# Optimization experiments

Measured on AMD Instinct MI355X. Metric: run time of the kernel, lower is better.

## Reference

```python
import jax, jax.numpy as jnp
import numpy as np
from jax import lax

DIM = 256
NUM_HEADS = 8
SW = 7
HEAD_DIM = DIM // NUM_HEADS
SCALE = HEAD_DIM ** -0.5


def setup_inputs() -> dict:
    key = jax.random.key(0)
    ks = jax.random.split(key, 7)
    B, C, H, W = 8, DIM, 56, 56
    x = jax.random.normal(ks[0], (B, C, H, W), dtype=jnp.float32)
    w_qkv = jax.random.normal(ks[1], (3 * C, C), dtype=jnp.float32) * 0.02
    b_qkv = jnp.zeros((3 * C,), dtype=jnp.float32)
    # depthwise 3x3 kernel, OIHW with feature_group_count=C -> (C,1,3,3)
    w_dw = jax.random.normal(ks[2], (C, 1, 3, 3), dtype=jnp.float32) * 0.02
    b_dw = jnp.zeros((C,), dtype=jnp.float32)
    w_proj = jax.random.normal(ks[3], (C, C), dtype=jnp.float32) * 0.02
    b_proj = jnp.zeros((C,), dtype=jnp.float32)
    return {"x": x, "w_qkv": w_qkv, "b_qkv": b_qkv, "w_dw": w_dw,
            "b_dw": b_dw, "w_proj": w_proj, "b_proj": b_proj}


def _conv1x1(x, w, b):
    # x:[B,C,H,W], w:[O,C] -> [B,O,H,W]
    return jnp.einsum('bchw,oc->bohw', x, w) + b[None, :, None, None]


def _dwconv3x3(x, w, b):
    C = x.shape[1]
    y = lax.conv_general_dilated(x, w, window_strides=(1, 1), padding='SAME',
                                 dimension_numbers=('NCHW', 'OIHW', 'NCHW'),
                                 feature_group_count=C)
    return y + b[None, :, None, None]


def _stripe_attn_H(q, k, v, sw):
    # q,k,v: [B,h,C,H,W]; local attention within sw-thick horizontal stripes
    B, h, C, H, W = q.shape
    sw = min(sw, H)
    pad = (-H) % sw
    if pad:
        pw = [(0, 0)] * 3 + [(0, pad), (0, 0)]
        q = jnp.pad(q, pw); k = jnp.pad(k, pw); v = jnp.pad(v, pw)
    Hp = H + pad
    n = Hp // sw

    def rs(t):
        # -> [B,h,n, sw*W, C]
        return t.reshape(B, h, C, n, sw, W).transpose(0, 1, 3, 4, 5, 2).reshape(B, h, n, sw * W, C)

    qs, ks_, vs = rs(q) * SCALE, rs(k), rs(v)
    attn = jax.nn.softmax(jnp.einsum('bhnqc,bhnkc->bhnqk', qs, ks_), axis=-1)
    out = jnp.einsum('bhnqk,bhnkc->bhnqc', attn, vs)
    out = out.reshape(B, h, n, sw, W, C).transpose(0, 1, 5, 2, 3, 4).reshape(B, h, C, Hp, W)
    return out[:, :, :, :H, :]


def _stripe_attn_W(q, k, v, sw):
    # attention within sw-thick vertical stripes; softmax is permutation-
    # equivariant over the stripe sequence, so transposing H<->W and reusing
    # the H-stripe kernel computes identical math.
    t = lambda a: a.transpose(0, 1, 2, 4, 3)
    return t(_stripe_attn_H(t(q), t(k), t(v), sw))


def reference(x, w_qkv, b_qkv, w_dw, b_dw, w_proj, b_proj):
    B, C, H, W = x.shape
    hh = NUM_HEADS // 2
    qkv = _conv1x1(x, w_qkv, b_qkv)
    q, k, v = jnp.split(qkv, 3, axis=1)
    v = v + _dwconv3x3(v, w_dw, b_dw)

    def heads(t):
        return t.reshape(B, NUM_HEADS, HEAD_DIM, H, W)

    q, k, v = heads(q), heads(k), heads(v)
    out_h = _stripe_attn_H(q[:, :hh], k[:, :hh], v[:, :hh], SW)
    out_w = _stripe_attn_W(q[:, hh:], k[:, hh:], v[:, hh:], SW)
    out = jnp.concatenate([out_h, out_w], axis=1).reshape(B, C, H, W)
    return _conv1x1(out, w_proj, b_proj)
```

## Files before the change

### kernel.cpp

```cpp
#include <hip/hip_runtime.h>
#include <hip/hip_bf16.h>
#include <stdint.h>

#define Bn 8
#define Cn 256
#define Hn 56
#define Wn 56
#define HWn 3136
#define NHEADS 8
#define HDIM 32
#define SEQ 392
#define NSTR 8
#define QKV_LD 768
#define KSC (0.17677669529663689f * 1.4426950408889634f)

#if __has_builtin(__builtin_amdgcn_exp2f)
#define EXP2(x) __builtin_amdgcn_exp2f(x)
#else
#define EXP2(x) exp2f(x)
#endif

typedef short short8 __attribute__((ext_vector_type(8)));
typedef float floatx4 __attribute__((ext_vector_type(4)));

__device__ __forceinline__ unsigned short f2bf(float f) {
  union { float f; uint32_t u; } v; v.f = f;
  uint32_t u = v.u;
  u += 0x7fffu + ((u >> 16) & 1u);
  return (unsigned short)(u >> 16);
}
__device__ __forceinline__ float bf2f(unsigned short h) {
  union { uint32_t u; float f; } v; v.u = ((uint32_t)h) << 16;
  return v.f;
}
__device__ __forceinline__ uint32_t cvt_pk_bf16(float lo, float hi) {
  uint32_t r;
  asm("v_cvt_pk_bf16_f32 %0, %1, %2" : "=v"(r) : "v"(lo), "v"(hi));
  return r;
}
__device__ __forceinline__ void gload16(const unsigned short* g, unsigned short* l) {
  __builtin_amdgcn_global_load_lds((const __attribute__((address_space(1))) void*)g,
                                   (__attribute__((address_space(3))) void*)l, 16, 0, 0);
}

__global__ __launch_bounds__(256) void k_cvt2(const float* __restrict__ a,
                                              const float* __restrict__ b2,
                                              unsigned short* __restrict__ da,
                                              unsigned short* __restrict__ db) {
  int i = blockIdx.x * 256 + threadIdx.x;
  if (i < 49152) {
    float4 v = ((const float4*)a)[i];
    ushort4 o;
    o.x = f2bf(v.x); o.y = f2bf(v.y); o.z = f2bf(v.z); o.w = f2bf(v.w);
    ((ushort4*)da)[i] = o;
  } else {
    int k = i - 49152;
    float4 v = ((const float4*)b2)[k];
    ushort4 o;
    o.x = f2bf(v.x); o.y = f2bf(v.y); o.z = f2bf(v.z); o.w = f2bf(v.w);
    ((ushort4*)db)[k] = o;
  }
}

__global__ __launch_bounds__(256) void k_trans_x(const float* __restrict__ x,
                                                 unsigned short* __restrict__ xt) {
  __shared__ float tile[32][33];
  int pb = blockIdx.x, cb = blockIdx.y, b = blockIdx.z;
  int t = threadIdx.x;
  int c = t >> 3, p4 = (t & 7) * 4;
  float4 v = *(const float4*)(x + (((size_t)b * Cn + cb * 32 + c) * HWn + pb * 32 + p4));
  tile[c][p4 + 0] = v.x; tile[c][p4 + 1] = v.y; tile[c][p4 + 2] = v.z; tile[c][p4 + 3] = v.w;
  __syncthreads();
  int p = t >> 3, c4 = (t & 7) * 4;
  ushort4 o;
  o.x = f2bf(tile[c4 + 0][p]); o.y = f2bf(tile[c4 + 1][p]);
  o.z = f2bf(tile[c4 + 2][p]); o.w = f2bf(tile[c4 + 3][p]);
  *(ushort4*)(xt + (((size_t)b * HWn + pb * 32 + p) * Cn + cb * 32 + c4)) = o;
}

template <int EPI>
__global__ __launch_bounds__(256) void k_gemm(const unsigned short* __restrict__ A,
                                              const unsigned short* __restrict__ Bt,
                                              const float* __restrict__ bias,
                                              unsigned short* __restrict__ outB,
                                              float* __restrict__ outF,
                                              unsigned short* __restrict__ qkvw,
                                              int M, int N, int K) {
  __shared__ __align__(16) unsigned short As[128 * 64];
  __shared__ __align__(16) unsigned short Bs[128 * 64];
  int t = threadIdx.x;
  int n0 = blockIdx.x * 128, m0 = blockIdx.y * 128;
  int b = blockIdx.z;
  const unsigned short* Bb = Bt + (size_t)b * N * K;
  int lane = t & 63, w = t >> 6;
  int wr = w >> 1, wc = w & 1;
  int g = lane >> 4, q = lane & 15;
  int srow = w * 32 + (lane >> 3);
  int slot = lane & 7;

  floatx4 z4 = {0.f, 0.f, 0.f, 0.f};
  floatx4 acc[4][4];
#pragma unroll
  for (int i = 0; i < 4; i++)
#pragma unroll
    for (int j = 0; j < 4; j++) acc[i][j] = z4;

  for (int k0 = 0; k0 < K; k0 += 64) {
    __syncthreads();
#pragma unroll
    for (int i = 0; i < 4; i++) {
      int row = srow + i * 8;
      int cs = slot ^ (row & 7);
      gload16(A + (size_t)(m0 + row) * K + k0 + cs * 8, &As[(w * 32 + i * 8) * 64]);
    }
#pragma unroll
    for (int i = 0; i < 4; i++) {
      int row = srow + i * 8;
      int cs = slot ^ (row & 7);
      int nr = n0 + row;
      if (nr < N)
        gload16(Bb + (size_t)nr * K + k0 + cs * 8, &Bs[(w * 32 + i * 8) * 64]);
    }
    asm volatile("s_waitcnt vmcnt(0)" ::: "memory");
    __syncthreads();
#pragma unroll
    for (int kk = 0; kk < 64; kk += 32) {
      short8 af[4], bfr[4];
#pragma unroll
      for (int i = 0; i < 4; i++) {
        int row = wr * 64 + i * 16 + q;
        af[i] = *(const short8*)&As[row * 64 + ((((kk >> 3) + g) ^ (q & 7)) << 3)];
      }
#pragma unroll
      for (int j = 0; j < 4; j++) {
        int row = wc * 64 + j * 16 + q;
        bfr[j] = *(const short8*)&Bs[row * 64 + ((((kk >> 3) + g) ^ (q & 7)) << 3)];
      }
#pragma unroll
      for (int i = 0; i < 4; i++)
#pragma unroll
        for (int j = 0; j < 4; j++)
          acc[i][j] = __builtin_amdgcn_mfma_f32_16x16x32_bf16(af[i], bfr[j], acc[i][j], 0, 0, 0);
    }
  }

#pragma unroll
  for (int i = 0; i < 4; i++) {
    int ob = m0 + wr * 64 + i * 16 + g * 4;
    float bs0 = bias[ob + 0], bs1 = bias[ob + 1], bs2 = bias[ob + 2], bs3 = bias[ob + 3];
    float sc = 1.0f;
    if (EPI == 0 && ob >= 256 && ob < 512) sc = KSC;
#pragma unroll
    for (int j = 0; j < 4; j++) {
      int col = n0 + wc * 64 + j * 16 + q;
      if (col < N) {
        if (EPI == 0) {
          ushort4 o;
          o.x = f2bf((acc[i][j][0] + bs0) * sc);
          o.y = f2bf((acc[i][j][1] + bs1) * sc);
          o.z = f2bf((acc[i][j][2] + bs2) * sc);
          o.w = f2bf((acc[i][j][3] + bs3) * sc);
          *(ushort4*)(outB + ((size_t)b * N + col) * M + ob) = o;
          int wch = -1;
          if (ob >= 128 && ob < 256) wch = ob - 128;
          else if (ob >= 384 && ob < 512) wch = ob - 384 + 128;
          if (wch >= 0) {
            int pw = (col % Wn) * Wn + col / Wn;
            *(ushort4*)(qkvw + ((size_t)b * HWn + pw) * 256 + wch) = o;
          }
        } else {
          float* po = outF + (size_t)b * M * N;
          po[(size_t)(ob + 0) * N + col] = acc[i][j][0] + bs0;
          po[(size_t)(ob + 1) * N + col] = acc[i][j][1] + bs1;
          po[(size_t)(ob + 2) * N + col] = acc[i][j][2] + bs2;
          po[(size_t)(ob + 3) * N + col] = acc[i][j][3] + bs3;
        }
      }
    }
  }
}

__global__ __launch_bounds__(256) void k_dwconv_t(const unsigned short* __restrict__ qkv,
                                                  const float* __restrict__ wdw,
                                                  const float* __restrict__ bdw,
                                                  unsigned short* __restrict__ vmt) {
  __shared__ float wS[1152];
  __shared__ float bS[128];
  __shared__ __align__(16) unsigned short tile[16][140];
  int t = threadIdx.x;
  int pass = blockIdx.y, b = blockIdx.z;
  for (int i = t; i < 1152; i += 256) wS[i] = wdw[pass * 1152 + i];
  if (t < 128) bS[t] = bdw[pass * 128 + t];
  __syncthreads();

  int pi = t >> 4, c8 = (t & 15) * 8;
  int i16 = blockIdx.x * 16 + pi;
  int h, w;
  if (pass == 0) { h = i16 / Wn; w = i16 % Wn; }
  else           { w = i16 / Hn; h = i16 % Hn; }

  const unsigned short* vq = qkv + 512 + pass * 128 + c8;
  float a[8];
  short8 vc = *(const short8*)(vq + ((size_t)b * HWn + h * Wn + w) * QKV_LD);
#pragma unroll
  for (int e = 0; e < 8; e++) a[e] = bf2f((unsigned short)vc[e]) + bS[c8 + e];
#pragma unroll
  for (int ky = 0; ky < 3; ky++) {
    int hh = h + ky - 1;
    if (hh < 0 || hh >= Hn) continue;
#pragma unroll
    for (int kx = 0; kx < 3; kx++) {
      int ww = w + kx - 1;
      if (ww < 0 || ww >= Wn) continue;
      short8 vn = *(const short8*)(vq + ((size_t)b * HWn + hh * Wn + ww) * QKV_LD);
#pragma unroll
      for (int e = 0; e < 8; e++) a[e] += bf2f((unsigned short)vn[e]) * wS[(c8 + e) * 9 + ky * 3 + kx];
    }
  }
  short8 o;
#pragma unroll
  for (int e = 0; e < 8; e++) o[e] = (short)f2bf(a[e]);
  *(short8*)&tile[pi][c8] = o;
  __syncthreads();

  int dd = t >> 1, half = t & 1;
  short8 ov;
#pragma unroll
  for (int k2 = 0; k2 < 8; k2++) ov[k2] = (short)tile[half * 8 + k2][dd];
  *(short8*)(vmt + ((size_t)(b * Cn + pass * 128 + dd)) * HWn + blockIdx.x * 16 + half * 8) = ov;
}

__global__ __launch_bounds__(256) void k_attn(const unsigned short* __restrict__ qkv,
                                              const unsigned short* __restrict__ qkvw,
                                              const unsigned short* __restrict__ vmt,
                                              unsigned short* __restrict__ aout) {
  __shared__ __align__(16) unsigned short Ks[12288];
  __shared__ __align__(16) unsigned short Vf[12800];
  __shared__ __align__(16) unsigned short Pf[2048];
  int s = blockIdx.x;
  int hd = blockIdx.y & 7, b = blockIdx.y >> 3;
  int part = blockIdx.z;
  int t = threadIdx.x, lane = t & 63, wv = t >> 6;
  bool wst = (hd >= 4);
  int q = lane & 15, g = lane >> 4;
  int sbase = s * SEQ;

  const unsigned short* base; int ld, qoff, koff;
  if (wst) { base = qkvw + (size_t)b * HWn * 256;    ld = 256;    qoff = (hd - 4) * 32; koff = 128 + (hd - 4) * 32; }
  else     { base = qkv  + (size_t)b * HWn * QKV_LD; ld = QKV_LD; qoff = hd * 32;       koff = 256 + hd * 32; }

  int qb0 = part * 13, qb1 = part ? 25 : 13;

  short8 qpre[4];
#pragma unroll
  for (int it = 0; it < 4; it++) {
    int qb = qb0 + wv + it * 4;
    int qi = qb * 16 + q;
    int qil = (qi < SEQ) ? qi : 391;
    qpre[it] = *(const short8*)(base + qoff + (size_t)(sbase + qil) * ld + g * 8);
  }

  const unsigned short* kgp = base + koff;
#pragma unroll
  for (int P = 0; P < 6; P++) {
    int key = P * 64 + wv * 16 + q;
    int gg = (t >> 4) & 3;
    short8 kv = *(const short8*)(kgp + (size_t)(sbase + key) * ld + gg * 8);
    *(short8*)&Ks[((((key >> 4) * 4 + gg) * 16) + (key & 15)) * 8] = kv;
  }
  short8 kf24;
  {
    int key = 384 + q; if (key > 391) key = 391;
    kf24 = *(const short8*)(kgp + (size_t)(sbase + key) * ld + g * 8);
  }
  const unsigned short* vg = vmt + ((size_t)(b * Cn + hd * HDIM)) * HWn + sbase;
  for (int idx = t; idx < 1600; idx += 256) {
    int d = idx / 50, Gc = idx % 50;
    short8 vv = *(const short8*)(vg + (size_t)d * HWn + Gc * 8);
    *(short8*)&Vf[(Gc * 32 + (d ^ (Gc & 7))) * 8] = vv;
  }
  __syncthreads();

  floatx4 z4 = {0.f, 0.f, 0.f, 0.f};
  unsigned short* Pw = &Pf[wv * 512];
  int gh = g >> 1, ge = (g & 1) * 4;

#pragma unroll
  for (int it = 0; it < 4; it++) {
    int qb = qb0 + wv + it * 4;
    if (qb >= qb1) continue;
    int qi = qb * 16 + q;
    int qil = (qi < SEQ) ? qi : 391;
    short8 qf = qpre[it];

    floatx4 sacc[25];
#pragma unroll
    for (int j = 0; j < 24; j++) {
      short8 kf = *(const short8*)&Ks[((j * 4 + g) * 16 + q) * 8];
      sacc[j] = __builtin_amdgcn_mfma_f32_16x16x32_bf16(kf, qf, z4, 0, 0, 0);
    }
    sacc[24] = __builtin_amdgcn_mfma_f32_16x16x32_bf16(kf24, qf, z4, 0, 0, 0);
    if (g >= 2) { sacc[24][0] = sacc[24][1] = sacc[24][2] = sacc[24][3] = -3.0e38f; }

    float sm = 0.f;
#pragma unroll
    for (int j = 0; j < 25; j++) {
      float e0 = EXP2(sacc[j][0]); float e1 = EXP2(sacc[j][1]);
      float e2 = EXP2(sacc[j][2]); float e3 = EXP2(sacc[j][3]);
      sacc[j][0] = e0; sacc[j][1] = e1; sacc[j][2] = e2; sacc[j][3] = e3;
      sm += (e0 + e1) + (e2 + e3);
    }
    sm += __shfl_xor(sm, 16);
    sm += __shfl_xor(sm, 32);
    float rcp = 1.0f / sm;

#define WRITEP(cc) do {                                                        \
    uint2 wA, wB;                                                              \
    wA.x = cvt_pk_bf16(sacc[2*(cc)][0], sacc[2*(cc)][1]);                      \
    wA.y = cvt_pk_bf16(sacc[2*(cc)][2], sacc[2*(cc)][3]);                      \
    if (2*(cc)+1 < 25) {                                                       \
      wB.x = cvt_pk_bf16(sacc[2*(cc)+1][0], sacc[2*(cc)+1][1]);                \
      wB.y = cvt_pk_bf16(sacc[2*(cc)+1][2], sacc[2*(cc)+1][3]);                \
    } else { wB.x = 0u; wB.y = 0u; }                                           \
    *(uint2*)&Pw[(gh * 16 + q) * 8 + ge] = wA;                                 \
    *(uint2*)&Pw[((2 + gh) * 16 + q) * 8 + ge] = wB;                           \
  } while (0)

    floatx4 o0 = z4, o1 = z4;
    WRITEP(0);
#pragma unroll
    for (int ch = 0; ch < 13; ch++) {
      asm volatile("s_waitcnt lgkmcnt(0)" ::: "memory");
      short8 pfr = *(const short8*)&Pw[(g * 16 + q) * 8];
      int Gc = ch * 4 + g; if (Gc > 49) Gc = 49;
      int sw = Gc & 7;
      short8 vf0 = *(const short8*)&Vf[(Gc * 32 + (q ^ sw)) * 8];
      short8 vf1 = *(const short8*)&Vf[(Gc * 32 + 16 + (q ^ sw)) * 8];
      if (ch < 12) {
        switch (ch + 1) {
          case 1: WRITEP(1); break;  case 2: WRITEP(2); break;
          case 3: WRITEP(3); break;  case 4: WRITEP(4); break;
          case 5: WRITEP(5); break;  case 6: WRITEP(6); break;
          case 7: WRITEP(7); break;  case 8: WRITEP(8); break;
          case 9: WRITEP(9); break;  case 10: WRITEP(10); break;
          case 11: WRITEP(11); break; case 12: WRITEP(12); break;
        }
      }
      o0 = __builtin_amdgcn_mfma_f32_16x16x32_bf16(vf0, pfr, o0, 0, 0, 0);
      o1 = __builtin_amdgcn_mfma_f32_16x16x32_bf16(vf1, pfr, o1, 0, 0, 0);
    }
#undef WRITEP

    if (qi < SEQ) {
      int pq = wst ? ((qil % Wn) * Wn + s * 7 + qil / Wn) : (sbase + qil);
      size_t ob = ((size_t)b * HWn + pq) * Cn + hd * HDIM;
      ushort4 u0, u1;
      u0.x = f2bf(o0[0] * rcp); u0.y = f2bf(o0[1] * rcp);
      u0.z = f2bf(o0[2] * rcp); u0.w = f2bf(o0[3] * rcp);
      u1.x = f2bf(o1[0] * rcp); u1.y = f2bf(o1[1] * rcp);
      u1.z = f2bf(o1[2] * rcp); u1.w = f2bf(o1[3] * rcp);
      *(ushort4*)(aout + ob + g * 4) = u0;
      *(ushort4*)(aout + ob + 16 + g * 4) = u1;
    }
  }
}

extern "C" void kernel_launch(void* const* d_in, const int* in_sizes, int n_in,
                              void* d_out, int out_size, void* d_ws, size_t ws_size,
                              hipStream_t stream) {
  const float* x     = (const float*)d_in[0];
  const float* wqkv  = (const float*)d_in[1];
  const float* bqkv  = (const float*)d_in[2];
  const float* wdw   = (const float*)d_in[3];
  const float* bdw   = (const float*)d_in[4];
  const float* wproj = (const float*)d_in[5];
  const float* bproj = (const float*)d_in[6];
  float* out = (float*)d_out;

  unsigned short* xt   = (unsigned short*)d_ws;
  unsigned short* wqb  = xt + (size_t)Bn * HWn * Cn;
  unsigned short* wpb  = wqb + 768 * 256;
  unsigned short* qkvb = wpb + 256 * 256;
  unsigned short* vmt  = qkvb + (size_t)Bn * HWn * QKV_LD;
  unsigned short* aout = vmt + (size_t)Bn * HWn * Cn;
  unsigned short* qkvw = aout + (size_t)Bn * HWn * Cn;

  k_cvt2<<<dim3(256), 256, 0, stream>>>(wqkv, wproj, wqb, wpb);
  k_trans_x<<<dim3(98, 8, Bn), 256, 0, stream>>>(x, xt);
  k_gemm<0><<<dim3(25, 6, Bn), 256, 0, stream>>>(wqb, xt, bqkv, qkvb, nullptr, qkvw, 768, HWn, 256);
  k_dwconv_t<<<dim3(196, 2, Bn), 256, 0, stream>>>(qkvb, wdw, bdw, vmt);
  k_attn<<<dim3(NSTR, Bn * NHEADS, 2), 256, 0, stream>>>(qkvb, qkvw, vmt, aout);
  k_gemm<1><<<dim3(25, 2, Bn), 256, 0, stream>>>(wpb, aout, bproj, nullptr, out, nullptr, 256, HWn, 256);
}
```

Baseline: 118.3 us.

## Double-buffer GEMM LDS, remap blocks across XCDs, move W-transposed copy to dwconv

```diff
diff --git a/kernel.cpp b/kernel.cpp
--- a/kernel.cpp
+++ b/kernel.cpp
@@ -84,13 +84,15 @@
                                               const float* __restrict__ bias,
                                               unsigned short* __restrict__ outB,
                                               float* __restrict__ outF,
-                                              unsigned short* __restrict__ qkvw,
-                                              int M, int N, int K) {
-  __shared__ __align__(16) unsigned short As[128 * 64];
-  __shared__ __align__(16) unsigned short Bs[128 * 64];
+                                              int M, int N, int K, int nx, int nper) {
+  __shared__ __align__(16) unsigned short As[2][128 * 64];
+  __shared__ __align__(16) unsigned short Bs[2][128 * 64];
   int t = threadIdx.x;
-  int n0 = blockIdx.x * 128, m0 = blockIdx.y * 128;
-  int b = blockIdx.z;
+  int raw = blockIdx.x;
+  int chunk = gridDim.x >> 3;
+  int wg = (raw & 7) * chunk + (raw >> 3);
+  int b = wg / nper, r = wg % nper;
+  int m0 = (r / nx) * 128, n0 = (r % nx) * 128;
   const unsigned short* Bb = Bt + (size_t)b * N * K;
   int lane = t & 63, w = t >> 6;
   int wr = w >> 1, wc = w & 1;
@@ -98,6 +100,21 @@
   int srow = w * 32 + (lane >> 3);
   int slot = lane & 7;
 
+  const unsigned short* Ag[4];
+  const unsigned short* Bg[4];
+  bool bok[4];
+  int ldst[4];
+#pragma unroll
+  for (int i = 0; i < 4; i++) {
+    int row = srow + i * 8;
+    int cs = slot ^ (row & 7);
+    Ag[i] = A + (size_t)(m0 + row) * K + cs * 8;
+    int nr = n0 + row;
+    bok[i] = (nr < N);
+    Bg[i] = Bb + (size_t)(bok[i] ? nr : (N - 1)) * K + cs * 8;
+    ldst[i] = (w * 32 + i * 8) * 64;
+  }
+
   floatx4 z4 = {0.f, 0.f, 0.f, 0.f};
   floatx4 acc[4][4];
 #pragma unroll
@@ -105,42 +122,45 @@
 #pragma unroll
     for (int j = 0; j < 4; j++) acc[i][j] = z4;
 
-  for (int k0 = 0; k0 < K; k0 += 64) {
-    __syncthreads();
-#pragma unroll
-    for (int i = 0; i < 4; i++) {
-      int row = srow + i * 8;
-      int cs = slot ^ (row & 7);
-      gload16(A + (size_t)(m0 + row) * K + k0 + cs * 8, &As[(w * 32 + i * 8) * 64]);
-    }
-#pragma unroll
-    for (int i = 0; i < 4; i++) {
-      int row = srow + i * 8;
-      int cs = slot ^ (row & 7);
-      int nr = n0 + row;
-      if (nr < N)
-        gload16(Bb + (size_t)nr * K + k0 + cs * 8, &Bs[(w * 32 + i * 8) * 64]);
-    }
-    asm volatile("s_waitcnt vmcnt(0)" ::: "memory");
-    __syncthreads();
+#pragma unroll
+  for (int i = 0; i < 4; i++) gload16(Ag[i], &As[0][ldst[i]]);
+#pragma unroll
+  for (int i = 0; i < 4; i++) if (bok[i]) gload16(Bg[i], &Bs[0][ldst[i]]);
+  asm volatile("s_waitcnt vmcnt(0)" ::: "memory");
+  __syncthreads();
+
+  int cur = 0;
+  for (int tt = 0; tt < 4; tt++) {
+    if (tt < 3) {
+      int k0 = (tt + 1) * 64;
+#pragma unroll
+      for (int i = 0; i < 4; i++) gload16(Ag[i] + k0, &As[cur ^ 1][ldst[i]]);
+#pragma unroll
+      for (int i = 0; i < 4; i++) if (bok[i]) gload16(Bg[i] + k0, &Bs[cur ^ 1][ldst[i]]);
+    }
 #pragma unroll
     for (int kk = 0; kk < 64; kk += 32) {
       short8 af[4], bfr[4];
 #pragma unroll
       for (int i = 0; i < 4; i++) {
         int row = wr * 64 + i * 16 + q;
-        af[i] = *(const short8*)&As[row * 64 + ((((kk >> 3) + g) ^ (q & 7)) << 3)];
+        af[i] = *(const short8*)&As[cur][row * 64 + ((((kk >> 3) + g) ^ (q & 7)) << 3)];
       }
 #pragma unroll
       for (int j = 0; j < 4; j++) {
         int row = wc * 64 + j * 16 + q;
-        bfr[j] = *(const short8*)&Bs[row * 64 + ((((kk >> 3) + g) ^ (q & 7)) << 3)];
+        bfr[j] = *(const short8*)&Bs[cur][row * 64 + ((((kk >> 3) + g) ^ (q & 7)) << 3)];
       }
 #pragma unroll
       for (int i = 0; i < 4; i++)
 #pragma unroll
         for (int j = 0; j < 4; j++)
           acc[i][j] = __builtin_amdgcn_mfma_f32_16x16x32_bf16(af[i], bfr[j], acc[i][j], 0, 0, 0);
+    }
+    if (tt < 3) {
+      asm volatile("s_waitcnt vmcnt(0)" ::: "memory");
+      __syncthreads();
+      cur ^= 1;
     }
   }
 
@@ -161,13 +181,6 @@
           o.z = f2bf((acc[i][j][2] + bs2) * sc);
           o.w = f2bf((acc[i][j][3] + bs3) * sc);
           *(ushort4*)(outB + ((size_t)b * N + col) * M + ob) = o;
-          int wch = -1;
-          if (ob >= 128 && ob < 256) wch = ob - 128;
-          else if (ob >= 384 && ob < 512) wch = ob - 384 + 128;
-          if (wch >= 0) {
-            int pw = (col % Wn) * Wn + col / Wn;
-            *(ushort4*)(qkvw + ((size_t)b * HWn + pw) * 256 + wch) = o;
-          }
         } else {
           float* po = outF + (size_t)b * M * N;
           po[(size_t)(ob + 0) * N + col] = acc[i][j][0] + bs0;
@@ -183,7 +196,8 @@
 __global__ __launch_bounds__(256) void k_dwconv_t(const unsigned short* __restrict__ qkv,
                                                   const float* __restrict__ wdw,
                                                   const float* __restrict__ bdw,
-                                                  unsigned short* __restrict__ vmt) {
+                                                  unsigned short* __restrict__ vmt,
+                                                  unsigned short* __restrict__ qkvw) {
   __shared__ float wS[1152];
   __shared__ float bS[128];
   __shared__ __align__(16) unsigned short tile[16][140];
@@ -191,13 +205,26 @@
   int pass = blockIdx.y, b = blockIdx.z;
   for (int i = t; i < 1152; i += 256) wS[i] = wdw[pass * 1152 + i];
   if (t < 128) bS[t] = bdw[pass * 128 + t];
-  __syncthreads();
 
   int pi = t >> 4, c8 = (t & 15) * 8;
   int i16 = blockIdx.x * 16 + pi;
   int h, w;
   if (pass == 0) { h = i16 / Wn; w = i16 % Wn; }
   else           { w = i16 / Hn; h = i16 % Hn; }
+
+  if (pass == 1) {
+    int pi2 = t >> 4, c16 = (t & 15) * 16;
+    int ib = blockIdx.x * 16 + pi2;
+    int w2 = ib / Hn, h2 = ib % Hn;
+    size_t src = ((size_t)b * HWn + h2 * Wn + w2) * QKV_LD;
+    int sch = (c16 < 128) ? (128 + c16) : (256 + c16);
+    short8 v0 = *(const short8*)(qkv + src + sch);
+    short8 v1 = *(const short8*)(qkv + src + sch + 8);
+    unsigned short* dst = qkvw + ((size_t)b * HWn + ib) * 256 + c16;
+    *(short8*)dst = v0;
+    *(short8*)(dst + 8) = v1;
+  }
+  __syncthreads();
 
   const unsigned short* vq = qkv + 512 + pass * 128 + c8;
   float a[8];
@@ -387,8 +414,8 @@
 
   k_cvt2<<<dim3(256), 256, 0, stream>>>(wqkv, wproj, wqb, wpb);
   k_trans_x<<<dim3(98, 8, Bn), 256, 0, stream>>>(x, xt);
-  k_gemm<0><<<dim3(25, 6, Bn), 256, 0, stream>>>(wqb, xt, bqkv, qkvb, nullptr, qkvw, 768, HWn, 256);
-  k_dwconv_t<<<dim3(196, 2, Bn), 256, 0, stream>>>(qkvb, wdw, bdw, vmt);
+  k_gemm<0><<<dim3(1200), 256, 0, stream>>>(wqb, xt, bqkv, qkvb, nullptr, 768, HWn, 256, 25, 150);
+  k_dwconv_t<<<dim3(196, 2, Bn), 256, 0, stream>>>(qkvb, wdw, bdw, vmt, qkvw);
   k_attn<<<dim3(NSTR, Bn * NHEADS, 2), 256, 0, stream>>>(qkvb, qkvw, vmt, aout);
-  k_gemm<1><<<dim3(25, 2, Bn), 256, 0, stream>>>(wpb, aout, bproj, nullptr, out, nullptr, 256, HWn, 256);
-}
+  k_gemm<1><<<dim3(400), 256, 0, stream>>>(wpb, aout, bproj, nullptr, out, 256, HWn, 256, 25, 50);
+}
```

Measured after the change: 109.6 us. 7.4% less time.
